# Kernel optimization log

Hardware: AMD Instinct MI355X
Metric: run time of the kernel (lower is better)

## Reference

```python
import jax, jax.numpy as jnp
import numpy as np

H, W = 480, 640
ICP_W = 10.0
N_ITER = 20
FTOL = 1e-3
XTOL = 1e-8
DIST_THR = 200.0 / 15.0
NORMAL_THR = 0.94


def _skew(w):
    z = jnp.zeros((), w.dtype)
    return jnp.stack([
        jnp.stack([z, -w[2], w[1]]),
        jnp.stack([w[2], z, -w[0]]),
        jnp.stack([-w[1], w[0], z]),
    ])


def _exp_se3(xi):
    # xi = (v, w); SE3 exponential map (lie_se3_to_SE3)
    v, w = xi[:3], xi[3:]
    th2 = jnp.sum(w * w)
    th = jnp.sqrt(th2)
    small = th < 1e-8
    ths = jnp.where(small, 1.0, th)
    A = jnp.where(small, 1.0 - th2 / 6.0, jnp.sin(ths) / ths)
    B = jnp.where(small, 0.5 - th2 / 24.0, (1.0 - jnp.cos(ths)) / (ths * ths))
    C = jnp.where(small, 1.0 / 6.0 - th2 / 120.0, (ths - jnp.sin(ths)) / (ths * ths * ths))
    Wx = _skew(w)
    W2 = Wx @ Wx
    R = jnp.eye(3, dtype=xi.dtype) + A * Wx + B * W2
    V = jnp.eye(3, dtype=xi.dtype) + B * Wx + C * W2
    t = V @ v
    T = jnp.eye(4, dtype=xi.dtype)
    T = T.at[:3, :3].set(R).at[:3, 3].set(t)
    return T


def _bilinear(img, u, v):
    # img [H,W]; u,v [N] float pixel coords
    u0 = jnp.floor(u)
    v0 = jnp.floor(v)
    du = u - u0
    dv = v - v0
    u0i = jnp.clip(u0.astype(jnp.int32), 0, W - 1)
    u1i = jnp.clip(u0i + 1, 0, W - 1)
    v0i = jnp.clip(v0.astype(jnp.int32), 0, H - 1)
    v1i = jnp.clip(v0i + 1, 0, H - 1)
    I00 = img[v0i, u0i]; I01 = img[v0i, u1i]
    I10 = img[v1i, u0i]; I11 = img[v1i, u1i]
    return (I00 * (1 - du) + I01 * du) * (1 - dv) + (I10 * (1 - du) + I11 * du) * dv


def _forward(depth_ref, normals_ref, gray_ref, gray_target, points_target, normals_target, intrinsics):
    dt = depth_ref.dtype
    fx, fy = intrinsics[0, 0], intrinsics[1, 1]
    cx, cy = intrinsics[0, 2], intrinsics[1, 2]
    vv, uu = jnp.meshgrid(jnp.arange(H, dtype=dt), jnp.arange(W, dtype=dt), indexing='ij')
    Z = depth_ref
    # ref PointCloud.from_depth: backprojection [N,3]
    P = jnp.stack([(uu - cx) / fx * Z, (vv - cy) / fy * Z, Z], -1).reshape(-1, 3)
    Nr = normals_ref.reshape(-1, 3)
    Ir = gray_ref.reshape(-1)
    gy_img, gx_img = jnp.gradient(gray_target)  # d/dv, d/du
    Nflt = jnp.asarray(H * W, dt)

    def step(carry, _):
        x, conv, cost = carry
        T = _exp_se3(x)
        R, t = T[:3, :3], T[:3, 3]
        Pt = P @ R.T + t  # transformed ref points [N,3]
        Zt = Pt[:, 2]
        okz = Zt > 1e-6
        Zs = jnp.where(okz, Zt, 1.0)
        u = fx * Pt[:, 0] / Zs + cx
        v = fy * Pt[:, 1] / Zs + cy
        inb = okz & (u >= 0) & (u <= W - 1) & (v >= 0) & (v <= H - 1)
        ui = jnp.clip(jnp.round(u).astype(jnp.int32), 0, W - 1)
        vi = jnp.clip(jnp.round(v).astype(jnp.int32), 0, H - 1)
        # --- ICP point-to-plane, projective association ---
        q = points_target[vi, ui]    # [N,3]
        nq = normals_target[vi, ui]  # [N,3]
        d = Pt - q
        nref_rot = Nr @ R.T
        valid_icp = inb & (jnp.sum(d * d, -1) < DIST_THR ** 2) & (jnp.sum(nref_rot * nq, -1) > NORMAL_THR)
        m_icp = valid_icp.astype(dt)
        r_icp = jnp.sum(nq * d, -1) * m_icp                              # [N]
        J_icp = jnp.concatenate([nq, jnp.cross(Pt, nq)], -1) * m_icp[:, None]  # [N,6]
        # --- RGB photometric ---
        m_rgb = inb.astype(dt)
        It = _bilinear(gray_target, u, v)
        r_rgb = (It - Ir) * m_rgb
        gxs = _bilinear(gx_img, u, v)
        gys = _bilinear(gy_img, u, v)
        # grad_I * d(projection)/d(point)
        gp = jnp.stack([
            gxs * fx / Zs,
            gys * fy / Zs,
            -(gxs * fx * Pt[:, 0] + gys * fy * Pt[:, 1]) / (Zs * Zs),
        ], -1)
        J_rgb = jnp.concatenate([gp, jnp.cross(Pt, gp)], -1) * m_rgb[:, None]
        # --- normal equations ---
        A = ICP_W * (J_icp.T @ J_icp) + J_rgb.T @ J_rgb
        b = ICP_W * (J_icp.T @ r_icp) + J_rgb.T @ r_rgb
        x0 = jnp.linalg.solve(A + 1e-9 * jnp.eye(6, dtype=dt), b)
        new_cost = ICP_W * jnp.sum(r_icp ** 2) / Nflt + jnp.sum(r_rgb ** 2) / Nflt
        c = conv | (new_cost < FTOL) | (jnp.linalg.norm(x0) < XTOL * (XTOL + jnp.linalg.norm(x)))
        x_new = jnp.where(c, x, x - x0)
        cost_new = jnp.where(conv, cost, new_cost)
        return (x_new, c, cost_new), None

    init = (jnp.zeros(6, dt), jnp.array(False), jnp.asarray(0.0, dt))
    (x, conv, cost), _ = jax.lax.scan(step, init, None, length=N_ITER)
    return _exp_se3(x), cost


def setup_inputs() -> dict:
    key = jax.random.key(0)
    ks = jax.random.split(key, 6)
    intrinsics = jnp.array([[525.0, 0.0, 319.5], [0.0, 525.0, 239.5], [0.0, 0.0, 1.0]], jnp.float32)
    fx, fy, cx, cy = 525.0, 525.0, 319.5, 239.5
    depth_ref = 0.5 + 1.5 * jax.random.uniform(ks[0], (H, W), jnp.float32)
    depth_t = 0.5 + 1.5 * jax.random.uniform(ks[1], (H, W), jnp.float32)
    vv, uu = jnp.meshgrid(jnp.arange(H, dtype=jnp.float32), jnp.arange(W, dtype=jnp.float32), indexing='ij')
    points_target = jnp.stack([(uu - cx) / fx * depth_t, (vv - cy) / fy * depth_t, depth_t], -1)
    def mk_normals(k):
        n = 0.1 * jax.random.normal(k, (H, W, 3), jnp.float32) + jnp.array([0.0, 0.0, -1.0])
        return n / jnp.linalg.norm(n, axis=-1, keepdims=True)
    normals_ref = mk_normals(ks[2])
    normals_target = mk_normals(ks[3])
    gray_ref = jax.random.uniform(ks[4], (H, W), jnp.float32)
    gray_target = jax.random.uniform(ks[5], (H, W), jnp.float32)
    return {
        'depth_ref': depth_ref,
        'normals_ref': normals_ref,
        'gray_ref': gray_ref,
        'gray_target': gray_target,
        'points_target': points_target,
        'normals_target': normals_target,
        'intrinsics': intrinsics,
    }


def reference(depth_ref, normals_ref, gray_ref, gray_target, points_target, normals_target, intrinsics):
    return _forward(depth_ref, normals_ref, gray_ref, gray_target, points_target, normals_target, intrinsics)
```

## Files before the change

### kernel.cpp

```cpp
#include <hip/hip_runtime.h>
#include <math.h>

#define HH 480
#define WW 640
#define NPIX (HH*WW)
#define NACC 29
#define TPB 256
#define PXPT 4
#define MB (NPIX/(TPB*PXPT))

#define WS_PART 32

__device__ __forceinline__ float gradu(const float* g, int v, int u) {
    const float* row = g + v * WW;
    if (u == 0)      return row[1] - row[0];
    if (u == WW - 1) return row[WW - 1] - row[WW - 2];
    return 0.5f * (row[u + 1] - row[u - 1]);
}
__device__ __forceinline__ float gradv(const float* g, int v, int u) {
    if (v == 0)      return g[WW + u] - g[u];
    if (v == HH - 1) return g[(HH - 1) * WW + u] - g[(HH - 2) * WW + u];
    return 0.5f * (g[(v + 1) * WW + u] - g[(v - 1) * WW + u]);
}

__device__ void exp_se3_f32(const float* xi, float* T) {
    float v0 = xi[0], v1 = xi[1], v2 = xi[2];
    float w0 = xi[3], w1 = xi[4], w2 = xi[5];
    float th2 = w0 * w0 + w1 * w1 + w2 * w2;
    float th = sqrtf(th2);
    bool small = th < 1e-8f;
    float ths = small ? 1.0f : th;
    float A = small ? (1.0f - th2 / 6.0f) : (sinf(ths) / ths);
    float B = small ? (0.5f - th2 / 24.0f) : ((1.0f - cosf(ths)) / (ths * ths));
    float C = small ? (1.0f / 6.0f - th2 / 120.0f) : ((ths - sinf(ths)) / (ths * ths * ths));
    float Wx[9] = { 0.f, -w2,  w1,
                    w2,  0.f, -w0,
                   -w1,  w0,  0.f };
    float W2[9];
    #pragma unroll
    for (int i = 0; i < 3; i++)
        #pragma unroll
        for (int j = 0; j < 3; j++) {
            float s = 0.f;
            #pragma unroll
            for (int k = 0; k < 3; k++) s += Wx[i * 3 + k] * Wx[k * 3 + j];
            W2[i * 3 + j] = s;
        }
    float R[9], V[9];
    #pragma unroll
    for (int i = 0; i < 9; i++) {
        float id = (i == 0 || i == 4 || i == 8) ? 1.0f : 0.0f;
        R[i] = id + A * Wx[i] + B * W2[i];
        V[i] = id + B * Wx[i] + C * W2[i];
    }
    float t0 = V[0] * v0 + V[1] * v1 + V[2] * v2;
    float t1 = V[3] * v0 + V[4] * v1 + V[5] * v2;
    float t2 = V[6] * v0 + V[7] * v1 + V[8] * v2;
    T[0] = R[0]; T[1] = R[1]; T[2]  = R[2]; T[3]  = t0;
    T[4] = R[3]; T[5] = R[4]; T[6]  = R[5]; T[7]  = t1;
    T[8] = R[6]; T[9] = R[7]; T[10] = R[8]; T[11] = t2;
    T[12] = 0.f; T[13] = 0.f; T[14] = 0.f; T[15] = 1.f;
}

__global__ void init_state(float* ws) {
    if (threadIdx.x == 0) {
        #pragma unroll
        for (int i = 0; i < 8; i++) ws[i] = 0.f;
        ws[8]  = 1.f; ws[9]  = 0.f; ws[10] = 0.f;
        ws[11] = 0.f; ws[12] = 1.f; ws[13] = 0.f;
        ws[14] = 0.f; ws[15] = 0.f; ws[16] = 1.f;
        ws[17] = 0.f; ws[18] = 0.f; ws[19] = 0.f;
    }
}

__device__ __forceinline__ void accum_point(float* acc, const float* J, float r, float w, int costslot) {
    int k = 0;
    #pragma unroll
    for (int i = 0; i < 6; i++) {
        #pragma unroll
        for (int j = i; j < 6; j++) { acc[k] += w * (J[i] * J[j]); k++; }
        acc[21 + i] += w * (J[i] * r);
    }
    acc[costslot] += r * r;
}

__device__ __forceinline__ void process_pixel(
    int p, float fx, float fy, float cx, float cy,
    float R00, float R01, float R02, float R10, float R11, float R12,
    float R20, float R21, float R22, float t0, float t1, float t2,
    const float* __restrict__ depth_ref, const float* __restrict__ normals_ref,
    const float* __restrict__ gray_ref, const float* __restrict__ gray_target,
    const float* __restrict__ points_target, const float* __restrict__ normals_target,
    float* acc)
{
    int vv = p / WW;
    int uu = p - vv * WW;

    float Z = depth_ref[p];
    float Px = ((float)uu - cx) / fx * Z;
    float Py = ((float)vv - cy) / fy * Z;
    float Pz = Z;
    float Ptx = R00 * Px + R01 * Py + R02 * Pz + t0;
    float Pty = R10 * Px + R11 * Py + R12 * Pz + t1;
    float Ptz = R20 * Px + R21 * Py + R22 * Pz + t2;
    bool okz = Ptz > 1e-6f;
    float Zs = okz ? Ptz : 1.0f;
    float u = fx * Ptx / Zs + cx;
    float v = fy * Pty / Zs + cy;
    bool inb = okz && (u >= 0.f) && (u <= (float)(WW - 1)) && (v >= 0.f) && (v <= (float)(HH - 1));
    if (!inb) return;

    int ui = (int)rintf(u); ui = ui < 0 ? 0 : (ui > WW - 1 ? WW - 1 : ui);
    int vi = (int)rintf(v); vi = vi < 0 ? 0 : (vi > HH - 1 ? HH - 1 : vi);
    int qi = (vi * WW + ui) * 3;
    float qx = points_target[qi], qy = points_target[qi + 1], qz = points_target[qi + 2];
    float nqx = normals_target[qi], nqy = normals_target[qi + 1], nqz = normals_target[qi + 2];
    float dx = Ptx - qx, dy = Pty - qy, dz = Ptz - qz;
    float nr0 = normals_ref[3 * p], nr1 = normals_ref[3 * p + 1], nr2 = normals_ref[3 * p + 2];
    float nrx = R00 * nr0 + R01 * nr1 + R02 * nr2;
    float nry = R10 * nr0 + R11 * nr1 + R12 * nr2;
    float nrz = R20 * nr0 + R21 * nr1 + R22 * nr2;
    const float DIST2 = (float)((200.0 / 15.0) * (200.0 / 15.0));
    if ((dx * dx + dy * dy + dz * dz) < DIST2 &&
        (nrx * nqx + nry * nqy + nrz * nqz) > 0.94f) {
        float r = nqx * dx + nqy * dy + nqz * dz;
        float J[6] = { nqx, nqy, nqz,
                       Pty * nqz - Ptz * nqy,
                       Ptz * nqx - Ptx * nqz,
                       Ptx * nqy - Pty * nqx };
        accum_point(acc, J, r, 10.0f, 27);
    }
    float u0f = floorf(u), v0f = floorf(v);
    float du = u - u0f, dv = v - v0f;
    int u0 = (int)u0f; u0 = u0 < 0 ? 0 : (u0 > WW - 1 ? WW - 1 : u0);
    int u1 = (u0 + 1 > WW - 1) ? WW - 1 : u0 + 1;
    int v0 = (int)v0f; v0 = v0 < 0 ? 0 : (v0 > HH - 1 ? HH - 1 : v0);
    int v1 = (v0 + 1 > HH - 1) ? HH - 1 : v0 + 1;
    const float* g = gray_target;
    float I00 = g[v0 * WW + u0], I01 = g[v0 * WW + u1];
    float I10 = g[v1 * WW + u0], I11 = g[v1 * WW + u1];
    float It  = (I00 * (1.f - du) + I01 * du) * (1.f - dv) + (I10 * (1.f - du) + I11 * du) * dv;
    float gx00 = gradu(g, v0, u0), gx01 = gradu(g, v0, u1);
    float gx10 = gradu(g, v1, u0), gx11 = gradu(g, v1, u1);
    float gxs = (gx00 * (1.f - du) + gx01 * du) * (1.f - dv) + (gx10 * (1.f - du) + gx11 * du) * dv;
    float gy00 = gradv(g, v0, u0), gy01 = gradv(g, v0, u1);
    float gy10 = gradv(g, v1, u0), gy11 = gradv(g, v1, u1);
    float gys = (gy00 * (1.f - du) + gy01 * du) * (1.f - dv) + (gy10 * (1.f - du) + gy11 * du) * dv;
    float rr = It - gray_ref[p];
    float gpx = gxs * fx / Zs;
    float gpy = gys * fy / Zs;
    float gpz = -(gxs * fx * Ptx + gys * fy * Pty) / (Zs * Zs);
    float J[6] = { gpx, gpy, gpz,
                   Pty * gpz - Ptz * gpy,
                   Ptz * gpx - Ptx * gpz,
                   Ptx * gpy - Pty * gpx };
    accum_point(acc, J, rr, 1.0f, 28);
}

__global__ __launch_bounds__(TPB) void map_reduce(
    const float* __restrict__ depth_ref,
    const float* __restrict__ normals_ref,
    const float* __restrict__ gray_ref,
    const float* __restrict__ gray_target,
    const float* __restrict__ points_target,
    const float* __restrict__ normals_target,
    const float* __restrict__ K,
    float* __restrict__ ws)
{
    const float fx = K[0], cx = K[2], fy = K[4], cy = K[5];
    const float R00 = ws[8],  R01 = ws[9],  R02 = ws[10];
    const float R10 = ws[11], R11 = ws[12], R12 = ws[13];
    const float R20 = ws[14], R21 = ws[15], R22 = ws[16];
    const float t0 = ws[17], t1 = ws[18], t2 = ws[19];

    float acc[NACC];
    #pragma unroll
    for (int i = 0; i < NACC; i++) acc[i] = 0.f;

    int pbase = blockIdx.x * (TPB * PXPT) + threadIdx.x;
    #pragma unroll
    for (int k = 0; k < PXPT; k++) {
        process_pixel(pbase + k * TPB, fx, fy, cx, cy,
                      R00, R01, R02, R10, R11, R12, R20, R21, R22, t0, t1, t2,
                      depth_ref, normals_ref, gray_ref, gray_target,
                      points_target, normals_target, acc);
    }

    #pragma unroll
    for (int q = 0; q < NACC; q++) {
        float vq = acc[q];
        #pragma unroll
        for (int off = 32; off >= 1; off >>= 1) vq += __shfl_xor(vq, off);
        acc[q] = vq;
    }
    __shared__ float lds[4][NACC];
    int wave = threadIdx.x >> 6;
    int lane = threadIdx.x & 63;
    if (lane == 0) {
        #pragma unroll
        for (int q = 0; q < NACC; q++) lds[wave][q] = acc[q];
    }
    __syncthreads();
    if (threadIdx.x < NACC) {
        int q = threadIdx.x;
        float s = lds[0][q] + lds[1][q] + lds[2][q] + lds[3][q];
        ws[WS_PART + q * MB + blockIdx.x] = s;
    }
}

__global__ __launch_bounds__(TPB) void solve_update(float* __restrict__ ws,
                                                    float* __restrict__ out,
                                                    int final_iter)
{
    __shared__ double part8[NACC * 8];
    __shared__ double sums[NACC];
    int tid = threadIdx.x;
    const float* part = ws + WS_PART;
    if (tid < NACC * 8) {
        int q = tid >> 3, s = tid & 7;
        const int CH = (MB + 7) / 8;
        int lo = s * CH;
        int hi = lo + CH; if (hi > MB) hi = MB;
        const float* row = part + q * MB;
        double a0 = 0.0, a1 = 0.0, a2 = 0.0, a3 = 0.0;
        int i = lo;
        for (; i + 4 <= hi; i += 4) {
            a0 += (double)row[i];
            a1 += (double)row[i + 1];
            a2 += (double)row[i + 2];
            a3 += (double)row[i + 3];
        }
        for (; i < hi; i++) a0 += (double)row[i];
        part8[tid] = ((a0 + a1) + (a2 + a3));
    }
    __syncthreads();
    if (tid < NACC) {
        double sm = 0.0;
        #pragma unroll
        for (int s = 0; s < 8; s++) sm += part8[tid * 8 + s];
        sums[tid] = sm;
    }
    __syncthreads();
    if (tid == 0) {
        double M[6][7];
        int k = 0;
        for (int i = 0; i < 6; i++)
            for (int j = i; j < 6; j++) { M[i][j] = sums[k]; M[j][i] = sums[k]; k++; }
        for (int i = 0; i < 6; i++) { M[i][6] = sums[21 + i]; M[i][i] += 1e-9; }
        double new_cost = 10.0 * sums[27] / (double)NPIX + sums[28] / (double)NPIX;

        for (int c = 0; c < 6; c++) {
            int piv = c; double mx = fabs(M[c][c]);
            for (int r2 = c + 1; r2 < 6; r2++) {
                double a = fabs(M[r2][c]);
                if (a > mx) { mx = a; piv = r2; }
            }
            if (piv != c)
                for (int j2 = 0; j2 < 7; j2++) { double tmp = M[c][j2]; M[c][j2] = M[piv][j2]; M[piv][j2] = tmp; }
            double inv = 1.0 / M[c][c];
            for (int r2 = c + 1; r2 < 6; r2++) {
                double f = M[r2][c] * inv;
                for (int j2 = c; j2 < 7; j2++) M[r2][j2] -= f * M[c][j2];
            }
        }
        double x0[6];
        for (int i = 5; i >= 0; i--) {
            double s = M[i][6];
            for (int j = i + 1; j < 6; j++) s -= M[i][j] * x0[j];
            x0[i] = s / M[i][i];
        }

        double nx0 = 0.0, nx = 0.0;
        float xf[6];
        for (int i = 0; i < 6; i++) {
            xf[i] = ws[i];
            nx0 += x0[i] * x0[i];
            nx  += (double)xf[i] * (double)xf[i];
        }
        nx0 = sqrt(nx0); nx = sqrt(nx);
        bool convold = (ws[6] != 0.f);
        bool c2 = convold || (new_cost < 1e-3) || (nx0 < 1e-8 * (1e-8 + nx));
        float xn[6];
        for (int i = 0; i < 6; i++)
            xn[i] = c2 ? xf[i] : (float)((double)xf[i] - x0[i]);
        for (int i = 0; i < 6; i++) ws[i] = xn[i];
        ws[6] = c2 ? 1.f : 0.f;
        if (!convold) ws[7] = (float)new_cost;

        float T[16];
        exp_se3_f32(xn, T);
        ws[8]  = T[0]; ws[9]  = T[1]; ws[10] = T[2];
        ws[11] = T[4]; ws[12] = T[5]; ws[13] = T[6];
        ws[14] = T[8]; ws[15] = T[9]; ws[16] = T[10];
        ws[17] = T[3]; ws[18] = T[7]; ws[19] = T[11];

        if (final_iter) {
            for (int i = 0; i < 16; i++) out[i] = T[i];
            out[16] = ws[7];
        }
    }
}

extern "C" void kernel_launch(void* const* d_in, const int* in_sizes, int n_in,
                              void* d_out, int out_size, void* d_ws, size_t ws_size,
                              hipStream_t stream) {
    const float* depth_ref      = (const float*)d_in[0];
    const float* normals_ref    = (const float*)d_in[1];
    const float* gray_ref       = (const float*)d_in[2];
    const float* gray_target    = (const float*)d_in[3];
    const float* points_target  = (const float*)d_in[4];
    const float* normals_target = (const float*)d_in[5];
    const float* K              = (const float*)d_in[6];
    float* ws  = (float*)d_ws;
    float* out = (float*)d_out;

    hipLaunchKernelGGL(init_state, dim3(1), dim3(64), 0, stream, ws);
    for (int it = 0; it < 20; ++it) {
        hipLaunchKernelGGL(map_reduce, dim3(MB), dim3(TPB), 0, stream,
                           depth_ref, normals_ref, gray_ref, gray_target,
                           points_target, normals_target, K, ws);
        hipLaunchKernelGGL(solve_update, dim3(1), dim3(TPB), 0, stream,
                           ws, out, (it == 19) ? 1 : 0);
    }
}
```

Baseline: 433.7 us.

## Fuse all ICP iterations into one persistent kernel with grid barriers

```diff
diff --git a/kernel.cpp b/kernel.cpp
--- a/kernel.cpp
+++ b/kernel.cpp
@@ -6,10 +6,15 @@
 #define NPIX (HH*WW)
 #define NACC 29
 #define TPB 256
-#define PXPT 4
-#define MB (NPIX/(TPB*PXPT))
-
-#define WS_PART 32
+#define PXPT 3
+#define MB 400
+
+#define WS_P0 64
+#define WS_P1 (WS_P0 + NACC*MB)
+#define WS_SMALL_END (WS_P1 + NACC*MB)
+#define WS_G4 23296
+#define WS_PN (WS_G4 + NPIX*4)
+#define WS_BIG_END (WS_PN + NPIX*8)
 
 __device__ __forceinline__ float gradu(const float* g, int v, int u) {
     const float* row = g + v * WW;
@@ -62,17 +67,6 @@
     T[12] = 0.f; T[13] = 0.f; T[14] = 0.f; T[15] = 1.f;
 }
 
-__global__ void init_state(float* ws) {
-    if (threadIdx.x == 0) {
-        #pragma unroll
-        for (int i = 0; i < 8; i++) ws[i] = 0.f;
-        ws[8]  = 1.f; ws[9]  = 0.f; ws[10] = 0.f;
-        ws[11] = 0.f; ws[12] = 1.f; ws[13] = 0.f;
-        ws[14] = 0.f; ws[15] = 0.f; ws[16] = 1.f;
-        ws[17] = 0.f; ws[18] = 0.f; ws[19] = 0.f;
-    }
-}
-
 __device__ __forceinline__ void accum_point(float* acc, const float* J, float r, float w, int costslot) {
     int k = 0;
     #pragma unroll
@@ -84,80 +78,27 @@
     acc[costslot] += r * r;
 }
 
-__device__ __forceinline__ void process_pixel(
-    int p, float fx, float fy, float cx, float cy,
-    float R00, float R01, float R02, float R10, float R11, float R12,
-    float R20, float R21, float R22, float t0, float t1, float t2,
-    const float* __restrict__ depth_ref, const float* __restrict__ normals_ref,
-    const float* __restrict__ gray_ref, const float* __restrict__ gray_target,
-    const float* __restrict__ points_target, const float* __restrict__ normals_target,
-    float* acc)
-{
-    int vv = p / WW;
-    int uu = p - vv * WW;
-
-    float Z = depth_ref[p];
-    float Px = ((float)uu - cx) / fx * Z;
-    float Py = ((float)vv - cy) / fy * Z;
-    float Pz = Z;
-    float Ptx = R00 * Px + R01 * Py + R02 * Pz + t0;
-    float Pty = R10 * Px + R11 * Py + R12 * Pz + t1;
-    float Ptz = R20 * Px + R21 * Py + R22 * Pz + t2;
-    bool okz = Ptz > 1e-6f;
-    float Zs = okz ? Ptz : 1.0f;
-    float u = fx * Ptx / Zs + cx;
-    float v = fy * Pty / Zs + cy;
-    bool inb = okz && (u >= 0.f) && (u <= (float)(WW - 1)) && (v >= 0.f) && (v <= (float)(HH - 1));
-    if (!inb) return;
-
-    int ui = (int)rintf(u); ui = ui < 0 ? 0 : (ui > WW - 1 ? WW - 1 : ui);
-    int vi = (int)rintf(v); vi = vi < 0 ? 0 : (vi > HH - 1 ? HH - 1 : vi);
-    int qi = (vi * WW + ui) * 3;
-    float qx = points_target[qi], qy = points_target[qi + 1], qz = points_target[qi + 2];
-    float nqx = normals_target[qi], nqy = normals_target[qi + 1], nqz = normals_target[qi + 2];
-    float dx = Ptx - qx, dy = Pty - qy, dz = Ptz - qz;
-    float nr0 = normals_ref[3 * p], nr1 = normals_ref[3 * p + 1], nr2 = normals_ref[3 * p + 2];
-    float nrx = R00 * nr0 + R01 * nr1 + R02 * nr2;
-    float nry = R10 * nr0 + R11 * nr1 + R12 * nr2;
-    float nrz = R20 * nr0 + R21 * nr1 + R22 * nr2;
-    const float DIST2 = (float)((200.0 / 15.0) * (200.0 / 15.0));
-    if ((dx * dx + dy * dy + dz * dz) < DIST2 &&
-        (nrx * nqx + nry * nqy + nrz * nqz) > 0.94f) {
-        float r = nqx * dx + nqy * dy + nqz * dz;
-        float J[6] = { nqx, nqy, nqz,
-                       Pty * nqz - Ptz * nqy,
-                       Ptz * nqx - Ptx * nqz,
-                       Ptx * nqy - Pty * nqx };
-        accum_point(acc, J, r, 10.0f, 27);
-    }
-    float u0f = floorf(u), v0f = floorf(v);
-    float du = u - u0f, dv = v - v0f;
-    int u0 = (int)u0f; u0 = u0 < 0 ? 0 : (u0 > WW - 1 ? WW - 1 : u0);
-    int u1 = (u0 + 1 > WW - 1) ? WW - 1 : u0 + 1;
-    int v0 = (int)v0f; v0 = v0 < 0 ? 0 : (v0 > HH - 1 ? HH - 1 : v0);
-    int v1 = (v0 + 1 > HH - 1) ? HH - 1 : v0 + 1;
-    const float* g = gray_target;
-    float I00 = g[v0 * WW + u0], I01 = g[v0 * WW + u1];
-    float I10 = g[v1 * WW + u0], I11 = g[v1 * WW + u1];
-    float It  = (I00 * (1.f - du) + I01 * du) * (1.f - dv) + (I10 * (1.f - du) + I11 * du) * dv;
-    float gx00 = gradu(g, v0, u0), gx01 = gradu(g, v0, u1);
-    float gx10 = gradu(g, v1, u0), gx11 = gradu(g, v1, u1);
-    float gxs = (gx00 * (1.f - du) + gx01 * du) * (1.f - dv) + (gx10 * (1.f - du) + gx11 * du) * dv;
-    float gy00 = gradv(g, v0, u0), gy01 = gradv(g, v0, u1);
-    float gy10 = gradv(g, v1, u0), gy11 = gradv(g, v1, u1);
-    float gys = (gy00 * (1.f - du) + gy01 * du) * (1.f - dv) + (gy10 * (1.f - du) + gy11 * du) * dv;
-    float rr = It - gray_ref[p];
-    float gpx = gxs * fx / Zs;
-    float gpy = gys * fy / Zs;
-    float gpz = -(gxs * fx * Ptx + gys * fy * Pty) / (Zs * Zs);
-    float J[6] = { gpx, gpy, gpz,
-                   Pty * gpz - Ptz * gpy,
-                   Ptz * gpx - Ptx * gpz,
-                   Ptx * gpy - Pty * gpx };
-    accum_point(acc, J, rr, 1.0f, 28);
-}
-
-__global__ __launch_bounds__(TPB) void map_reduce(
+__device__ __forceinline__ void grid_barrier(int* bar, int nb) {
+    __syncthreads();
+    if (threadIdx.x == 0) {
+        __threadfence();
+        int g = __hip_atomic_load(bar + 1, __ATOMIC_RELAXED, __HIP_MEMORY_SCOPE_AGENT);
+        int a = __hip_atomic_fetch_add(bar, 1, __ATOMIC_ACQ_REL, __HIP_MEMORY_SCOPE_AGENT);
+        if (a == nb - 1) {
+            __hip_atomic_store(bar, 0, __ATOMIC_RELAXED, __HIP_MEMORY_SCOPE_AGENT);
+            __hip_atomic_fetch_add(bar + 1, 1, __ATOMIC_RELEASE, __HIP_MEMORY_SCOPE_AGENT);
+        } else {
+            while (__hip_atomic_load(bar + 1, __ATOMIC_ACQUIRE, __HIP_MEMORY_SCOPE_AGENT) == g) {
+                __builtin_amdgcn_s_sleep(2);
+            }
+        }
+        __threadfence();
+    }
+    __syncthreads();
+}
+
+template <int PACKED>
+__global__ __launch_bounds__(TPB, 2) void fused_icp(
     const float* __restrict__ depth_ref,
     const float* __restrict__ normals_ref,
     const float* __restrict__ gray_ref,
@@ -165,139 +106,258 @@
     const float* __restrict__ points_target,
     const float* __restrict__ normals_target,
     const float* __restrict__ K,
-    float* __restrict__ ws)
+    float* __restrict__ ws,
+    float* __restrict__ out)
 {
+    const int tid = threadIdx.x;
+    const int bid = blockIdx.x;
     const float fx = K[0], cx = K[2], fy = K[4], cy = K[5];
-    const float R00 = ws[8],  R01 = ws[9],  R02 = ws[10];
-    const float R10 = ws[11], R11 = ws[12], R12 = ws[13];
-    const float R20 = ws[14], R21 = ws[15], R22 = ws[16];
-    const float t0 = ws[17], t1 = ws[18], t2 = ws[19];
-
-    float acc[NACC];
-    #pragma unroll
-    for (int i = 0; i < NACC; i++) acc[i] = 0.f;
-
-    int pbase = blockIdx.x * (TPB * PXPT) + threadIdx.x;
-    #pragma unroll
-    for (int k = 0; k < PXPT; k++) {
-        process_pixel(pbase + k * TPB, fx, fy, cx, cy,
-                      R00, R01, R02, R10, R11, R12, R20, R21, R22, t0, t1, t2,
-                      depth_ref, normals_ref, gray_ref, gray_target,
-                      points_target, normals_target, acc);
-    }
-
-    #pragma unroll
-    for (int q = 0; q < NACC; q++) {
-        float vq = acc[q];
-        #pragma unroll
-        for (int off = 32; off >= 1; off >>= 1) vq += __shfl_xor(vq, off);
-        acc[q] = vq;
-    }
+    int* bar = (int*)ws;
+    float4* g4 = (float4*)(ws + WS_G4);
+    float4* pn = (float4*)(ws + WS_PN);
+
+    if (PACKED) {
+        int base = bid * (TPB * PXPT) + tid;
+        #pragma unroll
+        for (int k = 0; k < PXPT; k++) {
+            int p = base + k * TPB;
+            int v = p / WW, u = p - v * WW;
+            float4 c;
+            c.x = gray_target[p];
+            c.y = gradu(gray_target, v, u);
+            c.z = gradv(gray_target, v, u);
+            c.w = 0.f;
+            g4[p] = c;
+            float4 a, b;
+            a.x = points_target[3 * p];
+            a.y = points_target[3 * p + 1];
+            a.z = points_target[3 * p + 2];
+            a.w = normals_target[3 * p];
+            b.x = normals_target[3 * p + 1];
+            b.y = normals_target[3 * p + 2];
+            b.z = 0.f; b.w = 0.f;
+            pn[2 * p] = a;
+            pn[2 * p + 1] = b;
+        }
+        grid_barrier(bar, MB);
+    }
+
+    __shared__ float sR[9], st_[3], sx[6];
+    __shared__ float sconv, scost;
     __shared__ float lds[4][NACC];
-    int wave = threadIdx.x >> 6;
-    int lane = threadIdx.x & 63;
-    if (lane == 0) {
-        #pragma unroll
-        for (int q = 0; q < NACC; q++) lds[wave][q] = acc[q];
-    }
-    __syncthreads();
-    if (threadIdx.x < NACC) {
-        int q = threadIdx.x;
-        float s = lds[0][q] + lds[1][q] + lds[2][q] + lds[3][q];
-        ws[WS_PART + q * MB + blockIdx.x] = s;
-    }
-}
-
-__global__ __launch_bounds__(TPB) void solve_update(float* __restrict__ ws,
-                                                    float* __restrict__ out,
-                                                    int final_iter)
-{
     __shared__ double part8[NACC * 8];
     __shared__ double sums[NACC];
-    int tid = threadIdx.x;
-    const float* part = ws + WS_PART;
-    if (tid < NACC * 8) {
-        int q = tid >> 3, s = tid & 7;
-        const int CH = (MB + 7) / 8;
-        int lo = s * CH;
-        int hi = lo + CH; if (hi > MB) hi = MB;
-        const float* row = part + q * MB;
-        double a0 = 0.0, a1 = 0.0, a2 = 0.0, a3 = 0.0;
-        int i = lo;
-        for (; i + 4 <= hi; i += 4) {
-            a0 += (double)row[i];
-            a1 += (double)row[i + 1];
-            a2 += (double)row[i + 2];
-            a3 += (double)row[i + 3];
-        }
-        for (; i < hi; i++) a0 += (double)row[i];
-        part8[tid] = ((a0 + a1) + (a2 + a3));
+
+    if (tid == 0) {
+        sR[0] = 1.f; sR[1] = 0.f; sR[2] = 0.f;
+        sR[3] = 0.f; sR[4] = 1.f; sR[5] = 0.f;
+        sR[6] = 0.f; sR[7] = 0.f; sR[8] = 1.f;
+        st_[0] = 0.f; st_[1] = 0.f; st_[2] = 0.f;
+        #pragma unroll
+        for (int i = 0; i < 6; i++) sx[i] = 0.f;
+        sconv = 0.f; scost = 0.f;
     }
     __syncthreads();
-    if (tid < NACC) {
-        double sm = 0.0;
-        #pragma unroll
-        for (int s = 0; s < 8; s++) sm += part8[tid * 8 + s];
-        sums[tid] = sm;
-    }
-    __syncthreads();
-    if (tid == 0) {
-        double M[6][7];
-        int k = 0;
-        for (int i = 0; i < 6; i++)
-            for (int j = i; j < 6; j++) { M[i][j] = sums[k]; M[j][i] = sums[k]; k++; }
-        for (int i = 0; i < 6; i++) { M[i][6] = sums[21 + i]; M[i][i] += 1e-9; }
-        double new_cost = 10.0 * sums[27] / (double)NPIX + sums[28] / (double)NPIX;
-
-        for (int c = 0; c < 6; c++) {
-            int piv = c; double mx = fabs(M[c][c]);
-            for (int r2 = c + 1; r2 < 6; r2++) {
-                double a = fabs(M[r2][c]);
-                if (a > mx) { mx = a; piv = r2; }
-            }
-            if (piv != c)
-                for (int j2 = 0; j2 < 7; j2++) { double tmp = M[c][j2]; M[c][j2] = M[piv][j2]; M[piv][j2] = tmp; }
-            double inv = 1.0 / M[c][c];
-            for (int r2 = c + 1; r2 < 6; r2++) {
-                double f = M[r2][c] * inv;
-                for (int j2 = c; j2 < 7; j2++) M[r2][j2] -= f * M[c][j2];
-            }
-        }
-        double x0[6];
-        for (int i = 5; i >= 0; i--) {
-            double s = M[i][6];
-            for (int j = i + 1; j < 6; j++) s -= M[i][j] * x0[j];
-            x0[i] = s / M[i][i];
-        }
-
-        double nx0 = 0.0, nx = 0.0;
-        float xf[6];
-        for (int i = 0; i < 6; i++) {
-            xf[i] = ws[i];
-            nx0 += x0[i] * x0[i];
-            nx  += (double)xf[i] * (double)xf[i];
-        }
-        nx0 = sqrt(nx0); nx = sqrt(nx);
-        bool convold = (ws[6] != 0.f);
-        bool c2 = convold || (new_cost < 1e-3) || (nx0 < 1e-8 * (1e-8 + nx));
-        float xn[6];
-        for (int i = 0; i < 6; i++)
-            xn[i] = c2 ? xf[i] : (float)((double)xf[i] - x0[i]);
-        for (int i = 0; i < 6; i++) ws[i] = xn[i];
-        ws[6] = c2 ? 1.f : 0.f;
-        if (!convold) ws[7] = (float)new_cost;
-
-        float T[16];
-        exp_se3_f32(xn, T);
-        ws[8]  = T[0]; ws[9]  = T[1]; ws[10] = T[2];
-        ws[11] = T[4]; ws[12] = T[5]; ws[13] = T[6];
-        ws[14] = T[8]; ws[15] = T[9]; ws[16] = T[10];
-        ws[17] = T[3]; ws[18] = T[7]; ws[19] = T[11];
-
-        if (final_iter) {
-            for (int i = 0; i < 16; i++) out[i] = T[i];
-            out[16] = ws[7];
-        }
+
+    for (int it = 0; it < 20; ++it) {
+        const float R00 = sR[0], R01 = sR[1], R02 = sR[2];
+        const float R10 = sR[3], R11 = sR[4], R12 = sR[5];
+        const float R20 = sR[6], R21 = sR[7], R22 = sR[8];
+        const float t0 = st_[0], t1 = st_[1], t2 = st_[2];
+
+        float acc[NACC];
+        #pragma unroll
+        for (int i = 0; i < NACC; i++) acc[i] = 0.f;
+
+        int pbase = bid * (TPB * PXPT) + tid;
+        #pragma unroll
+        for (int kk = 0; kk < PXPT; kk++) {
+            int p = pbase + kk * TPB;
+            int vv = p / WW;
+            int uu = p - vv * WW;
+
+            float Z = depth_ref[p];
+            float Px = ((float)uu - cx) / fx * Z;
+            float Py = ((float)vv - cy) / fy * Z;
+            float Pz = Z;
+            float Ptx = R00 * Px + R01 * Py + R02 * Pz + t0;
+            float Pty = R10 * Px + R11 * Py + R12 * Pz + t1;
+            float Ptz = R20 * Px + R21 * Py + R22 * Pz + t2;
+            bool okz = Ptz > 1e-6f;
+            float Zs = okz ? Ptz : 1.0f;
+            float u = fx * Ptx / Zs + cx;
+            float v = fy * Pty / Zs + cy;
+            bool inb = okz && (u >= 0.f) && (u <= (float)(WW - 1)) && (v >= 0.f) && (v <= (float)(HH - 1));
+            if (!inb) continue;
+
+            int ui = (int)rintf(u); ui = ui < 0 ? 0 : (ui > WW - 1 ? WW - 1 : ui);
+            int vi = (int)rintf(v); vi = vi < 0 ? 0 : (vi > HH - 1 ? HH - 1 : vi);
+            int ti = vi * WW + ui;
+            float qx, qy, qz, nqx, nqy, nqz;
+            if (PACKED) {
+                float4 a = pn[2 * ti], b = pn[2 * ti + 1];
+                qx = a.x; qy = a.y; qz = a.z; nqx = a.w; nqy = b.x; nqz = b.y;
+            } else {
+                qx = points_target[3 * ti]; qy = points_target[3 * ti + 1]; qz = points_target[3 * ti + 2];
+                nqx = normals_target[3 * ti]; nqy = normals_target[3 * ti + 1]; nqz = normals_target[3 * ti + 2];
+            }
+            float dx = Ptx - qx, dy = Pty - qy, dz = Ptz - qz;
+            float nr0 = normals_ref[3 * p], nr1 = normals_ref[3 * p + 1], nr2 = normals_ref[3 * p + 2];
+            float nrx = R00 * nr0 + R01 * nr1 + R02 * nr2;
+            float nry = R10 * nr0 + R11 * nr1 + R12 * nr2;
+            float nrz = R20 * nr0 + R21 * nr1 + R22 * nr2;
+            const float DIST2 = (float)((200.0 / 15.0) * (200.0 / 15.0));
+            if ((dx * dx + dy * dy + dz * dz) < DIST2 &&
+                (nrx * nqx + nry * nqy + nrz * nqz) > 0.94f) {
+                float r = nqx * dx + nqy * dy + nqz * dz;
+                float J[6] = { nqx, nqy, nqz,
+                               Pty * nqz - Ptz * nqy,
+                               Ptz * nqx - Ptx * nqz,
+                               Ptx * nqy - Pty * nqx };
+                accum_point(acc, J, r, 10.0f, 27);
+            }
+            float u0f = floorf(u), v0f = floorf(v);
+            float du = u - u0f, dv = v - v0f;
+            int u0 = (int)u0f; u0 = u0 < 0 ? 0 : (u0 > WW - 1 ? WW - 1 : u0);
+            int u1 = (u0 + 1 > WW - 1) ? WW - 1 : u0 + 1;
+            int v0 = (int)v0f; v0 = v0 < 0 ? 0 : (v0 > HH - 1 ? HH - 1 : v0);
+            int v1 = (v0 + 1 > HH - 1) ? HH - 1 : v0 + 1;
+            int i00 = v0 * WW + u0, i01 = v0 * WW + u1, i10 = v1 * WW + u0, i11 = v1 * WW + u1;
+            float I00, I01, I10, I11, gx00, gx01, gx10, gx11, gy00, gy01, gy10, gy11;
+            if (PACKED) {
+                float4 c00 = g4[i00], c01 = g4[i01], c10 = g4[i10], c11 = g4[i11];
+                I00 = c00.x; gx00 = c00.y; gy00 = c00.z;
+                I01 = c01.x; gx01 = c01.y; gy01 = c01.z;
+                I10 = c10.x; gx10 = c10.y; gy10 = c10.z;
+                I11 = c11.x; gx11 = c11.y; gy11 = c11.z;
+            } else {
+                const float* g = gray_target;
+                I00 = g[i00]; I01 = g[i01]; I10 = g[i10]; I11 = g[i11];
+                gx00 = gradu(g, v0, u0); gx01 = gradu(g, v0, u1);
+                gx10 = gradu(g, v1, u0); gx11 = gradu(g, v1, u1);
+                gy00 = gradv(g, v0, u0); gy01 = gradv(g, v0, u1);
+                gy10 = gradv(g, v1, u0); gy11 = gradv(g, v1, u1);
+            }
+            float It  = (I00 * (1.f - du) + I01 * du) * (1.f - dv) + (I10 * (1.f - du) + I11 * du) * dv;
+            float gxs = (gx00 * (1.f - du) + gx01 * du) * (1.f - dv) + (gx10 * (1.f - du) + gx11 * du) * dv;
+            float gys = (gy00 * (1.f - du) + gy01 * du) * (1.f - dv) + (gy10 * (1.f - du) + gy11 * du) * dv;
+            float rr = It - gray_ref[p];
+            float gpx = gxs * fx / Zs;
+            float gpy = gys * fy / Zs;
+            float gpz = -(gxs * fx * Ptx + gys * fy * Pty) / (Zs * Zs);
+            float J[6] = { gpx, gpy, gpz,
+                           Pty * gpz - Ptz * gpy,
+                           Ptz * gpx - Ptx * gpz,
+                           Ptx * gpy - Pty * gpx };
+            accum_point(acc, J, rr, 1.0f, 28);
+        }
+
+        #pragma unroll
+        for (int q = 0; q < NACC; q++) {
+            float vq = acc[q];
+            #pragma unroll
+            for (int off = 32; off >= 1; off >>= 1) vq += __shfl_xor(vq, off);
+            acc[q] = vq;
+        }
+        int wave = tid >> 6;
+        int lane = tid & 63;
+        __syncthreads();
+        if (lane == 0) {
+            #pragma unroll
+            for (int q = 0; q < NACC; q++) lds[wave][q] = acc[q];
+        }
+        __syncthreads();
+        float* pbuf = ws + ((it & 1) ? WS_P1 : WS_P0);
+        if (tid < NACC) {
+            int q = tid;
+            float s = lds[0][q] + lds[1][q] + lds[2][q] + lds[3][q];
+            pbuf[q * MB + bid] = s;
+        }
+        grid_barrier(bar, MB);
+
+        if (tid < NACC * 8) {
+            int q = tid >> 3, s = tid & 7;
+            const int CH = MB / 8;
+            int lo = s * CH, hi = lo + CH;
+            const float* row = pbuf + q * MB;
+            double a0 = 0.0, a1 = 0.0, a2 = 0.0, a3 = 0.0;
+            int i = lo;
+            for (; i + 4 <= hi; i += 4) {
+                a0 += (double)row[i];
+                a1 += (double)row[i + 1];
+                a2 += (double)row[i + 2];
+                a3 += (double)row[i + 3];
+            }
+            for (; i < hi; i++) a0 += (double)row[i];
+            part8[tid] = ((a0 + a1) + (a2 + a3));
+        }
+        __syncthreads();
+        if (tid < NACC) {
+            double sm = 0.0;
+            #pragma unroll
+            for (int s = 0; s < 8; s++) sm += part8[tid * 8 + s];
+            sums[tid] = sm;
+        }
+        __syncthreads();
+        if (tid == 0) {
+            double M[6][7];
+            int k = 0;
+            for (int i = 0; i < 6; i++)
+                for (int j = i; j < 6; j++) { M[i][j] = sums[k]; M[j][i] = sums[k]; k++; }
+            for (int i = 0; i < 6; i++) { M[i][6] = sums[21 + i]; M[i][i] += 1e-9; }
+            double new_cost = 10.0 * sums[27] / (double)NPIX + sums[28] / (double)NPIX;
+
+            for (int c = 0; c < 6; c++) {
+                int piv = c; double mx = fabs(M[c][c]);
+                for (int r2 = c + 1; r2 < 6; r2++) {
+                    double a = fabs(M[r2][c]);
+                    if (a > mx) { mx = a; piv = r2; }
+                }
+                if (piv != c)
+                    for (int j2 = 0; j2 < 7; j2++) { double tmp = M[c][j2]; M[c][j2] = M[piv][j2]; M[piv][j2] = tmp; }
+                double inv = 1.0 / M[c][c];
+                for (int r2 = c + 1; r2 < 6; r2++) {
+                    double f = M[r2][c] * inv;
+                    for (int j2 = c; j2 < 7; j2++) M[r2][j2] -= f * M[c][j2];
+                }
+            }
+            double x0[6];
+            for (int i = 5; i >= 0; i--) {
+                double s = M[i][6];
+                for (int j = i + 1; j < 6; j++) s -= M[i][j] * x0[j];
+                x0[i] = s / M[i][i];
+            }
+
+            double nx0 = 0.0, nx = 0.0;
+            float xf[6];
+            for (int i = 0; i < 6; i++) {
+                xf[i] = sx[i];
+                nx0 += x0[i] * x0[i];
+                nx  += (double)xf[i] * (double)xf[i];
+            }
+            nx0 = sqrt(nx0); nx = sqrt(nx);
+            bool convold = (sconv != 0.f);
+            bool c2 = convold || (new_cost < 1e-3) || (nx0 < 1e-8 * (1e-8 + nx));
+            float xn[6];
+            for (int i = 0; i < 6; i++)
+                xn[i] = c2 ? xf[i] : (float)((double)xf[i] - x0[i]);
+            for (int i = 0; i < 6; i++) sx[i] = xn[i];
+            sconv = c2 ? 1.f : 0.f;
+            if (!convold) scost = (float)new_cost;
+
+            float T[16];
+            exp_se3_f32(xn, T);
+            sR[0] = T[0]; sR[1] = T[1]; sR[2] = T[2];
+            sR[3] = T[4]; sR[4] = T[5]; sR[5] = T[6];
+            sR[6] = T[8]; sR[7] = T[9]; sR[8] = T[10];
+            st_[0] = T[3]; st_[1] = T[7]; st_[2] = T[11];
+
+            if (it == 19 && bid == 0) {
+                for (int i = 0; i < 16; i++) out[i] = T[i];
+                out[16] = scost;
+            }
+        }
+        __syncthreads();
     }
 }
 
@@ -314,12 +374,16 @@
     float* ws  = (float*)d_ws;
     float* out = (float*)d_out;
 
-    hipLaunchKernelGGL(init_state, dim3(1), dim3(64), 0, stream, ws);
-    for (int it = 0; it < 20; ++it) {
-        hipLaunchKernelGGL(map_reduce, dim3(MB), dim3(TPB), 0, stream,
+    hipMemsetAsync(d_ws, 0, 256, stream);
+
+    bool big = ws_size >= (size_t)WS_BIG_END * sizeof(float);
+    if (big) {
+        hipLaunchKernelGGL((fused_icp<1>), dim3(MB), dim3(TPB), 0, stream,
                            depth_ref, normals_ref, gray_ref, gray_target,
-                           points_target, normals_target, K, ws);
-        hipLaunchKernelGGL(solve_update, dim3(1), dim3(TPB), 0, stream,
-                           ws, out, (it == 19) ? 1 : 0);
-    }
-}
+                           points_target, normals_target, K, ws, out);
+    } else {
+        hipLaunchKernelGGL((fused_icp<0>), dim3(MB), dim3(TPB), 0, stream,
+                           depth_ref, normals_ref, gray_ref, gray_target,
+                           points_target, normals_target, K, ws, out);
+    }
+}
```

Result: slower. 1.716 ms (+295.6%).
